# Optimization experiments

Hardware: AMD Instinct MI355X
Metric: run time of the kernel (lower is better)

Reference implementation:

```python
import jax, jax.numpy as jnp
import numpy as np

E = 4096      # hidden_size
H = 32        # num_attention_heads
D = E // H    # head_dim = 128
PAST = 8191   # past kv length


def setup_inputs() -> dict:
    key = jax.random.key(0)
    ks = jax.random.split(key, 10)
    s = 0.02
    return {
        "hidden_states": jax.random.normal(ks[0], (1, 1, E), jnp.float32),
        "past_key": jax.random.normal(ks[1], (1, D, PAST), jnp.float32),
        "past_value": jax.random.normal(ks[2], (1, PAST, D), jnp.float32),
        "attention_mask": jnp.zeros((1, 1, 1, PAST + 1), jnp.float32),
        "q_w": jax.random.normal(ks[3], (E, E), jnp.float32) * s,
        "q_b": jnp.zeros((E,), jnp.float32),
        "kv_w": jax.random.normal(ks[4], (E, 2 * D), jnp.float32) * s,
        "kv_b": jnp.zeros((2 * D,), jnp.float32),
        "proj_w": jax.random.normal(ks[5], (E, E), jnp.float32) * s,
        "proj_b": jnp.zeros((E,), jnp.float32),
    }


def reference(hidden_states, past_key, past_value, attention_mask,
              q_w, q_b, kv_w, kv_b, proj_w, proj_b):
    B, S = hidden_states.shape[:2]  # B=1, S=1 (decode)
    # Conv1D projections: x @ W + b
    query = hidden_states @ q_w + q_b            # [B, S, E]
    kv = hidden_states @ kv_w + kv_b             # [B, S, 2D]
    key_new, value_new = kv[..., :D], kv[..., D:]  # [B, S, D] each

    q = query.reshape(B, S, H, D).transpose(0, 2, 1, 3)  # [B, H, S, D]
    key_perm = key_new.transpose(0, 2, 1)                 # [B, D, S]
    full_key = jnp.concatenate([past_key, key_perm], axis=-1)     # [B, D, K]
    full_value = jnp.concatenate([past_value, value_new], axis=-2)  # [B, K, D]
    K = full_key.shape[-1]

    # QK^T with shared single KV head, scaled by sqrt(head_dim)
    scores = jnp.einsum('bhqd,bdk->bhqk', q, full_key)  # [B, H, S, K]
    scores = scores / jnp.asarray(D ** 0.5, scores.dtype)

    # causal mask over rows [K-S, K)
    causal = (jnp.arange(K)[None, :] <= (jnp.arange(S) + (K - S))[:, None])  # [S, K]
    mask_value = jnp.asarray(jnp.finfo(scores.dtype).min, scores.dtype)
    scores = jnp.where(causal[None, None], scores, mask_value)
    scores = scores + attention_mask

    attn_weights = jax.nn.softmax(scores, axis=-1)                # [B, H, S, K]
    attn_out = jnp.einsum('bhqk,bkd->bhqd', attn_weights, full_value)  # [B, H, S, D]
    attn_out = attn_out.transpose(0, 2, 1, 3).reshape(B, S, E)    # merge heads
    attn_out = attn_out @ proj_w + proj_b                          # [B, S, E]
    return attn_out, key_perm, value_new
```

## Files before the change

### kernel.cpp

```cpp
#include <hip/hip_runtime.h>
#include <math.h>

#define E_DIM 4096
#define H_NUM 32
#define D_DIM 128
#define PAST_K 8191
#define K_TOT 8192

#define WS_QUERY 0
#define WS_KV    4096
#define WS_PQ    4608
#define WS_PA    (WS_PQ + 256*4352)
#define WS_PL    (WS_PA + 128*4096)
#define WS_PP    (WS_PL + 4096)

__global__ void __launch_bounds__(512, 2)
k_qkv(const float* __restrict__ hs,
      const float* __restrict__ q_w,
      const float* __restrict__ kv_w,
      float* __restrict__ ws) {
    const int t = threadIdx.x;
    const int e0 = blockIdx.y * 16;
    if (blockIdx.x < 2) {
        const int o = blockIdx.x * 2048 + t * 4;
        float ax = 0.f, ay = 0.f, az = 0.f, aw = 0.f;
#pragma unroll
        for (int i = 0; i < 16; ++i) {
            const int e = e0 + i;
            const float x = hs[e];
            const float4 w = *reinterpret_cast<const float4*>(q_w + (size_t)e * E_DIM + o);
            ax += x * w.x; ay += x * w.y; az += x * w.z; aw += x * w.w;
        }
        *reinterpret_cast<float4*>(ws + WS_PQ + (size_t)blockIdx.y * 4352 + o) =
            make_float4(ax, ay, az, aw);
    } else {
        if (t >= 64) return;
        const int o = t * 4;
        float ax = 0.f, ay = 0.f, az = 0.f, aw = 0.f;
#pragma unroll
        for (int i = 0; i < 16; ++i) {
            const int e = e0 + i;
            const float x = hs[e];
            const float4 w = *reinterpret_cast<const float4*>(kv_w + (size_t)e * 256 + o);
            ax += x * w.x; ay += x * w.y; az += x * w.z; aw += x * w.w;
        }
        *reinterpret_cast<float4*>(ws + WS_PQ + (size_t)blockIdx.y * 4352 + 4096 + o) =
            make_float4(ax, ay, az, aw);
    }
}

__global__ void __launch_bounds__(256, 4)
k_qkv_reduce(const float* __restrict__ q_b, const float* __restrict__ kv_b,
             float* __restrict__ ws, float* __restrict__ out) {
    __shared__ float rr[256];
    const int t = threadIdx.x;
    const int ol = t & 31;
    const int sg = t >> 5;
    const int o = blockIdx.x * 32 + ol;
    float acc = 0.f;
#pragma unroll 8
    for (int s = sg * 32; s < sg * 32 + 32; ++s)
        acc += ws[WS_PQ + (size_t)s * 4352 + o];
    rr[t] = acc;
    __syncthreads();
    if (t < 32) {
        float v = 0.f;
#pragma unroll
        for (int g = 0; g < 8; ++g) v += rr[g * 32 + t];
        const int oo = blockIdx.x * 32 + t;
        if (oo < 4096) {
            ws[WS_QUERY + oo] = v + q_b[oo];
        } else {
            const int i = oo - 4096;
            const float r = v + kv_b[i];
            ws[WS_KV + i] = r;
            out[oo] = r;
        }
    }
}

__global__ void __launch_bounds__(512, 2)
k_attn(const float* __restrict__ past_key,
       const float* __restrict__ past_value,
       const float* __restrict__ mask,
       float* __restrict__ ws) {
    __shared__ float sq[8 * 128];
    __shared__ float sp[8 * 64];
    __shared__ float red[3584];
    const int t = threadIdx.x;
    const int hy = blockIdx.y;
    const int kx = blockIdx.x;
    const int h0 = hy * 8;
    const int k0 = kx * 64;
    const float* __restrict__ kvn = ws + WS_KV;

    sq[t]       = ws[WS_QUERY + h0 * D_DIM + t];
    sq[t + 512] = ws[WS_QUERY + h0 * D_DIM + t + 512];
    __syncthreads();

    const int kl = t & 63;
    const int team = t >> 6;
    const int d0 = team * 16;
    const int k = k0 + kl;
    const bool tailA = (k == PAST_K);
    const float* kp = tailA ? (kvn + d0) : (past_key + (size_t)d0 * PAST_K + k);
    const size_t kstr = tailA ? 1 : PAST_K;

    float acc[8];
#pragma unroll
    for (int h = 0; h < 8; ++h) acc[h] = 0.f;

#pragma unroll
    for (int i = 0; i < 16; i += 4) {
        const float v0 = kp[0];
        const float v1 = kp[kstr];
        const float v2 = kp[2 * kstr];
        const float v3 = kp[3 * kstr];
        kp += 4 * kstr;
#pragma unroll
        for (int h = 0; h < 8; ++h) {
            const float4 q = *reinterpret_cast<const float4*>(&sq[h * 128 + d0 + i]);
            acc[h] += q.x * v0 + q.y * v1 + q.z * v2 + q.w * v3;
        }
    }
    if (team != 0) {
#pragma unroll
        for (int h = 0; h < 8; ++h)
            red[((team - 1) * 8 + h) * 64 + kl] = acc[h];
    }
    __syncthreads();
    if (team == 0) {
        const float scale = 0.08838834764831845f;
        const float mk = mask[k];
        float l[8];
#pragma unroll
        for (int h = 0; h < 8; ++h) {
            float s = acc[h];
#pragma unroll
            for (int tm = 0; tm < 7; ++tm) s += red[(tm * 8 + h) * 64 + kl];
            const float e = __expf(s * scale + mk);
            sp[h * 64 + kl] = e;
            l[h] = e;
        }
#pragma unroll
        for (int h = 0; h < 8; ++h) {
#pragma unroll
            for (int off = 32; off > 0; off >>= 1) l[h] += __shfl_xor(l[h], off);
        }
        if (t == 0) {
            float* pl = ws + WS_PL + ((size_t)(kx * 4 + hy)) * 8;
#pragma unroll
            for (int h = 0; h < 8; ++h) pl[h] = l[h];
        }
    }
    __syncthreads();

    const int d = t & 127;
    const int kg = t >> 7;
    const int kb = k0 + kg * 16;
    const float* __restrict__ vp = past_value + (size_t)kb * D_DIM + d;
    const float* __restrict__ vlast =
        (kb + 15 == PAST_K) ? (kvn + D_DIM + d) : (vp + 15 * (size_t)D_DIM);

    float b[8];
#pragma unroll
    for (int h = 0; h < 8; ++h) b[h] = 0.f;

#pragma unroll
    for (int kk = 0; kk < 15; ++kk) {
        const float v = vp[(size_t)kk * D_DIM];
#pragma unroll
        for (int h = 0; h < 8; ++h) b[h] += sp[h * 64 + kg * 16 + kk] * v;
    }
    {
        const float v = *vlast;
#pragma unroll
        for (int h = 0; h < 8; ++h) b[h] += sp[h * 64 + kg * 16 + 15] * v;
    }
    __syncthreads();
    if (kg != 0) {
#pragma unroll
        for (int h = 0; h < 8; ++h)
            red[((kg - 1) * 8 + h) * 128 + d] = b[h];
    }
    __syncthreads();
    if (kg == 0) {
#pragma unroll
        for (int h = 0; h < 8; ++h) {
            float s = b[h] + red[(0 * 8 + h) * 128 + d] +
                      red[(1 * 8 + h) * 128 + d] + red[(2 * 8 + h) * 128 + d];
            ws[WS_PA + (size_t)kx * 4096 + (h0 + h) * D_DIM + d] = s;
        }
    }
}

__global__ void __launch_bounds__(512, 2)
k_proj(const float* __restrict__ proj_w,
       float* __restrict__ ws) {
    __shared__ float sred[32 * 16];
    __shared__ float lpart[2];
    __shared__ float sa[16];
    const int t = threadIdx.x;
    const int by = blockIdx.y;
    const int e0 = by * 16;
    const int h  = by >> 3;

    {
        const int el = t & 15;
        const int kg = t >> 4;
        float ps = 0.f;
#pragma unroll
        for (int j = 0; j < 4; ++j)
            ps += ws[WS_PA + (size_t)(kg * 4 + j) * 4096 + e0 + el];
        sred[kg * 16 + el] = ps;
    }
    if (t < 128) {
        float lv = ws[WS_PL + (size_t)t * 32 + (h >> 3) * 8 + (h & 7)];
#pragma unroll
        for (int off = 32; off > 0; off >>= 1) lv += __shfl_xor(lv, off);
        if ((t & 63) == 0) lpart[t >> 6] = lv;
    }
    __syncthreads();
    if (t < 16) {
        float asum = 0.f;
#pragma unroll
        for (int g = 0; g < 32; ++g) asum += sred[g * 16 + t];
        sa[t] = asum / (lpart[0] + lpart[1]);
    }
    __syncthreads();

    const int o = blockIdx.x * 2048 + t * 4;
    float ax = 0.f, ay = 0.f, az = 0.f, aw = 0.f;
#pragma unroll
    for (int i = 0; i < 16; ++i) {
        const float x = sa[i];
        const float4 w = *reinterpret_cast<const float4*>(proj_w + (size_t)(e0 + i) * E_DIM + o);
        ax += x * w.x; ay += x * w.y; az += x * w.z; aw += x * w.w;
    }
    *reinterpret_cast<float4*>(ws + WS_PP + (size_t)by * 4096 + o) =
        make_float4(ax, ay, az, aw);
}

__global__ void __launch_bounds__(256, 4)
k_proj_reduce(const float* __restrict__ proj_b,
              float* __restrict__ ws, float* __restrict__ out) {
    __shared__ float rr[256];
    const int t = threadIdx.x;
    const int ol = t & 31;
    const int sg = t >> 5;
    const int o = blockIdx.x * 32 + ol;
    float acc = 0.f;
#pragma unroll 8
    for (int s = sg * 32; s < sg * 32 + 32; ++s)
        acc += ws[WS_PP + (size_t)s * 4096 + o];
    rr[t] = acc;
    __syncthreads();
    if (t < 32) {
        float v = 0.f;
#pragma unroll
        for (int g = 0; g < 8; ++g) v += rr[g * 32 + t];
        const int oo = blockIdx.x * 32 + t;
        out[oo] = v + proj_b[oo];
    }
}

extern "C" void kernel_launch(void* const* d_in, const int* in_sizes, int n_in,
                              void* d_out, int out_size, void* d_ws, size_t ws_size,
                              hipStream_t stream) {
    const float* hs      = (const float*)d_in[0];
    const float* past_k  = (const float*)d_in[1];
    const float* past_v  = (const float*)d_in[2];
    const float* mask    = (const float*)d_in[3];
    const float* q_w     = (const float*)d_in[4];
    const float* q_b     = (const float*)d_in[5];
    const float* kv_w    = (const float*)d_in[6];
    const float* kv_b    = (const float*)d_in[7];
    const float* proj_w  = (const float*)d_in[8];
    const float* proj_b  = (const float*)d_in[9];
    float* out = (float*)d_out;
    float* ws  = (float*)d_ws;

    k_qkv        <<<dim3(3, 256), dim3(512), 0, stream>>>(hs, q_w, kv_w, ws);
    k_qkv_reduce <<<dim3(136),    dim3(256), 0, stream>>>(q_b, kv_b, ws, out);
    k_attn       <<<dim3(128, 4), dim3(512), 0, stream>>>(past_k, past_v, mask, ws);
    k_proj       <<<dim3(2, 256), dim3(512), 0, stream>>>(proj_w, ws);
    k_proj_reduce<<<dim3(128),    dim3(256), 0, stream>>>(proj_b, ws, out);
}
```

Before: 193.4 us.

## Fold kv projection into q blocks, vectorize reductions, spread attention reductions across all threads

The qkv kernel drops its third, mostly idle grid column and instead gives the first block column 64 extra threads that compute the kv projection. Both split-K reduce kernels now load float4 partials across 32 segment groups of 8 rows, replacing scalar loads over 8 groups of 32. In the attention kernel, the softmax and PV cross-team reductions are shared by all eight teams (one head each) and by all four k-groups, instead of being serialized on one team, which also removes a barrier. The cost is more shared memory in attention and odd 576-thread blocks in qkv.

Result: faster. 187.3 us (-3.2%).

```diff
diff --git a/kernel.cpp b/kernel.cpp
--- a/kernel.cpp
+++ b/kernel.cpp
@@ -6,6 +6,8 @@
 #define D_DIM 128
 #define PAST_K 8191
 #define K_TOT 8192
+
+typedef float f32x4 __attribute__((ext_vector_type(4)));
 
 #define WS_QUERY 0
 #define WS_KV    4096
@@ -14,14 +16,14 @@
 #define WS_PL    (WS_PA + 128*4096)
 #define WS_PP    (WS_PL + 4096)
 
-__global__ void __launch_bounds__(512, 2)
+__global__ void __launch_bounds__(576, 2)
 k_qkv(const float* __restrict__ hs,
       const float* __restrict__ q_w,
       const float* __restrict__ kv_w,
       float* __restrict__ ws) {
     const int t = threadIdx.x;
     const int e0 = blockIdx.y * 16;
-    if (blockIdx.x < 2) {
+    if (t < 512) {
         const int o = blockIdx.x * 2048 + t * 4;
         float ax = 0.f, ay = 0.f, az = 0.f, aw = 0.f;
 #pragma unroll
@@ -33,9 +35,8 @@
         }
         *reinterpret_cast<float4*>(ws + WS_PQ + (size_t)blockIdx.y * 4352 + o) =
             make_float4(ax, ay, az, aw);
-    } else {
-        if (t >= 64) return;
-        const int o = t * 4;
+    } else if (blockIdx.x == 0) {
+        const int o = (t - 512) * 4;
         float ax = 0.f, ay = 0.f, az = 0.f, aw = 0.f;
 #pragma unroll
         for (int i = 0; i < 16; ++i) {
@@ -52,29 +53,33 @@
 __global__ void __launch_bounds__(256, 4)
 k_qkv_reduce(const float* __restrict__ q_b, const float* __restrict__ kv_b,
              float* __restrict__ ws, float* __restrict__ out) {
-    __shared__ float rr[256];
-    const int t = threadIdx.x;
-    const int ol = t & 31;
-    const int sg = t >> 5;
-    const int o = blockIdx.x * 32 + ol;
-    float acc = 0.f;
-#pragma unroll 8
-    for (int s = sg * 32; s < sg * 32 + 32; ++s)
-        acc += ws[WS_PQ + (size_t)s * 4352 + o];
-    rr[t] = acc;
-    __syncthreads();
-    if (t < 32) {
-        float v = 0.f;
-#pragma unroll
-        for (int g = 0; g < 8; ++g) v += rr[g * 32 + t];
-        const int oo = blockIdx.x * 32 + t;
+    __shared__ f32x4 rr[32][8];
+    const int t = threadIdx.x;
+    const int ol = t & 7;
+    const int sg = t >> 3;
+    const int o = blockIdx.x * 32 + ol * 4;
+    f32x4 acc = {0.f, 0.f, 0.f, 0.f};
+#pragma unroll
+    for (int s = sg * 8; s < sg * 8 + 8; ++s)
+        acc += *reinterpret_cast<const f32x4*>(ws + WS_PQ + (size_t)s * 4352 + o);
+    rr[sg][ol] = acc;
+    __syncthreads();
+    if (t < 8) {
+        f32x4 v = {0.f, 0.f, 0.f, 0.f};
+#pragma unroll
+        for (int g = 0; g < 32; ++g) v += rr[g][t];
+        const int oo = blockIdx.x * 32 + t * 4;
         if (oo < 4096) {
-            ws[WS_QUERY + oo] = v + q_b[oo];
+#pragma unroll
+            for (int j = 0; j < 4; ++j) ws[WS_QUERY + oo + j] = v[j] + q_b[oo + j];
         } else {
             const int i = oo - 4096;
-            const float r = v + kv_b[i];
-            ws[WS_KV + i] = r;
-            out[oo] = r;
+#pragma unroll
+            for (int j = 0; j < 4; ++j) {
+                const float r = v[j] + kv_b[i + j];
+                ws[WS_KV + i + j] = r;
+                out[oo + j] = r;
+            }
         }
     }
 }
@@ -86,7 +91,7 @@
        float* __restrict__ ws) {
     __shared__ float sq[8 * 128];
     __shared__ float sp[8 * 64];
-    __shared__ float red[3584];
+    __shared__ float red[4096];
     const int t = threadIdx.x;
     const int hy = blockIdx.y;
     const int kx = blockIdx.x;
@@ -123,35 +128,24 @@
             acc[h] += q.x * v0 + q.y * v1 + q.z * v2 + q.w * v3;
         }
     }
-    if (team != 0) {
-#pragma unroll
-        for (int h = 0; h < 8; ++h)
-            red[((team - 1) * 8 + h) * 64 + kl] = acc[h];
-    }
-    __syncthreads();
-    if (team == 0) {
+#pragma unroll
+    for (int h = 0; h < 8; ++h)
+        red[(team * 8 + h) * 64 + kl] = acc[h];
+    __syncthreads();
+
+    {
         const float scale = 0.08838834764831845f;
         const float mk = mask[k];
-        float l[8];
-#pragma unroll
-        for (int h = 0; h < 8; ++h) {
-            float s = acc[h];
-#pragma unroll
-            for (int tm = 0; tm < 7; ++tm) s += red[(tm * 8 + h) * 64 + kl];
-            const float e = __expf(s * scale + mk);
-            sp[h * 64 + kl] = e;
-            l[h] = e;
-        }
-#pragma unroll
-        for (int h = 0; h < 8; ++h) {
-#pragma unroll
-            for (int off = 32; off > 0; off >>= 1) l[h] += __shfl_xor(l[h], off);
-        }
-        if (t == 0) {
-            float* pl = ws + WS_PL + ((size_t)(kx * 4 + hy)) * 8;
-#pragma unroll
-            for (int h = 0; h < 8; ++h) pl[h] = l[h];
-        }
+        float s = 0.f;
+#pragma unroll
+        for (int tp = 0; tp < 8; ++tp) s += red[(tp * 8 + team) * 64 + kl];
+        const float e = __expf(s * scale + mk);
+        sp[team * 64 + kl] = e;
+        float l = e;
+#pragma unroll
+        for (int off = 32; off > 0; off >>= 1) l += __shfl_xor(l, off);
+        if (kl == 0)
+            ws[WS_PL + ((size_t)(kx * 4 + hy)) * 8 + team] = l;
     }
     __syncthreads();
 
@@ -177,20 +171,17 @@
 #pragma unroll
         for (int h = 0; h < 8; ++h) b[h] += sp[h * 64 + kg * 16 + 15] * v;
     }
-    __syncthreads();
-    if (kg != 0) {
-#pragma unroll
-        for (int h = 0; h < 8; ++h)
-            red[((kg - 1) * 8 + h) * 128 + d] = b[h];
-    }
-    __syncthreads();
-    if (kg == 0) {
-#pragma unroll
-        for (int h = 0; h < 8; ++h) {
-            float s = b[h] + red[(0 * 8 + h) * 128 + d] +
-                      red[(1 * 8 + h) * 128 + d] + red[(2 * 8 + h) * 128 + d];
-            ws[WS_PA + (size_t)kx * 4096 + (h0 + h) * D_DIM + d] = s;
-        }
+#pragma unroll
+    for (int h = 0; h < 8; ++h)
+        red[(kg * 8 + h) * 128 + d] = b[h];
+    __syncthreads();
+
+#pragma unroll
+    for (int j = 0; j < 2; ++j) {
+        const int hh = kg * 2 + j;
+        const float s = red[(0 * 8 + hh) * 128 + d] + red[(1 * 8 + hh) * 128 + d] +
+                        red[(2 * 8 + hh) * 128 + d] + red[(3 * 8 + hh) * 128 + d];
+        ws[WS_PA + (size_t)kx * 4096 + (h0 + hh) * D_DIM + d] = s;
     }
 }
 
@@ -244,23 +235,24 @@
 __global__ void __launch_bounds__(256, 4)
 k_proj_reduce(const float* __restrict__ proj_b,
               float* __restrict__ ws, float* __restrict__ out) {
-    __shared__ float rr[256];
-    const int t = threadIdx.x;
-    const int ol = t & 31;
-    const int sg = t >> 5;
-    const int o = blockIdx.x * 32 + ol;
-    float acc = 0.f;
-#pragma unroll 8
-    for (int s = sg * 32; s < sg * 32 + 32; ++s)
-        acc += ws[WS_PP + (size_t)s * 4096 + o];
-    rr[t] = acc;
-    __syncthreads();
-    if (t < 32) {
-        float v = 0.f;
-#pragma unroll
-        for (int g = 0; g < 8; ++g) v += rr[g * 32 + t];
-        const int oo = blockIdx.x * 32 + t;
-        out[oo] = v + proj_b[oo];
+    __shared__ f32x4 rr[32][8];
+    const int t = threadIdx.x;
+    const int ol = t & 7;
+    const int sg = t >> 3;
+    const int o = blockIdx.x * 32 + ol * 4;
+    f32x4 acc = {0.f, 0.f, 0.f, 0.f};
+#pragma unroll
+    for (int s = sg * 8; s < sg * 8 + 8; ++s)
+        acc += *reinterpret_cast<const f32x4*>(ws + WS_PP + (size_t)s * 4096 + o);
+    rr[sg][ol] = acc;
+    __syncthreads();
+    if (t < 8) {
+        f32x4 v = {0.f, 0.f, 0.f, 0.f};
+#pragma unroll
+        for (int g = 0; g < 32; ++g) v += rr[g][t];
+        const int oo = blockIdx.x * 32 + t * 4;
+        const f32x4 bb = *reinterpret_cast<const f32x4*>(proj_b + oo);
+        *reinterpret_cast<f32x4*>(out + oo) = v + bb;
     }
 }
 
@@ -280,7 +272,7 @@
     float* out = (float*)d_out;
     float* ws  = (float*)d_ws;
 
-    k_qkv        <<<dim3(3, 256), dim3(512), 0, stream>>>(hs, q_w, kv_w, ws);
+    k_qkv        <<<dim3(2, 256), dim3(576), 0, stream>>>(hs, q_w, kv_w, ws);
     k_qkv_reduce <<<dim3(136),    dim3(256), 0, stream>>>(q_b, kv_b, ws, out);
     k_attn       <<<dim3(128, 4), dim3(512), 0, stream>>>(past_k, past_v, mask, ws);
     k_proj       <<<dim3(2, 256), dim3(512), 0, stream>>>(proj_w, ws);
```
